# Kernel optimization log

Measured on AMD Instinct MI355X. Metric: run time of the kernel, lower is better.

The kernel has to match this reference:

```python
import jax, jax.numpy as jnp
import numpy as np

# Fixed architecture constants (from DMGHAN.__init__ / Mamba defaults)
D_MODEL = 256; D_STATE = 16; D_CONV = 4; D_INNER = 512; DT_RANK = 16
EMBED = 1024; N_CLASSES = [5, 30, 80, 200, 600, 1500]
B, L = 8, 2048


def setup_inputs() -> dict:
    key = jax.random.key(0)
    ks = jax.random.split(key, 32)
    def p(i, shape, s=0.02):
        return jax.random.normal(ks[i], shape, jnp.float32) * s
    inp = {
        "x": jax.random.normal(ks[0], (B, L, EMBED), jnp.float32),
        # input_proj
        "W_proj": p(1, (D_MODEL, EMBED)), "b_proj": p(2, (D_MODEL,)),
        # Mamba block params
        "W_in": p(3, (2 * D_INNER, D_MODEL)),
        "conv_w": p(4, (D_INNER, 1, D_CONV), 0.1), "conv_b": p(5, (D_INNER,), 0.1),
        "W_xp": p(6, (DT_RANK + 2 * D_STATE, D_INNER)),
        "W_dt": p(7, (D_INNER, DT_RANK), 0.1), "b_dt": p(8, (D_INNER,), 0.1),
        "A_log": jnp.log(jnp.broadcast_to(jnp.arange(1., D_STATE + 1., dtype=jnp.float32), (D_INNER, D_STATE))),
        "Dp": jnp.ones((D_INNER,), jnp.float32),
        "W_out": p(9, (D_MODEL, D_INNER)),
        # 6 MultiheadAttention layers (in_proj packed [q;k;v], out_proj)
        "mha_in_w": p(10, (6, 3 * D_MODEL, D_MODEL)), "mha_in_b": p(11, (6, 3 * D_MODEL)),
        "mha_out_w": p(12, (6, D_MODEL, D_MODEL)), "mha_out_b": p(13, (6, D_MODEL)),
        # 5 gates: Linear(512, 256) + sigmoid
        "gate_w": p(14, (5, D_MODEL, 2 * D_MODEL)), "gate_b": p(15, (5, D_MODEL)),
    }
    for i, nc in enumerate(N_CLASSES):
        inp[f"Wc{i}"] = p(16 + i, (nc, D_MODEL))
        inp[f"bc{i}"] = p(22 + i, (nc,))
    return inp


def mamba_block(x, W_in, conv_w, conv_b, W_xp, W_dt, b_dt, A_log, Dp, W_out):
    # x: (B, L, D_MODEL)
    u, z = jnp.split(x @ W_in.T, 2, axis=-1)          # each (B, L, D_INNER)
    # causal depthwise conv over time
    uc = jax.lax.conv_general_dilated(
        u.transpose(0, 2, 1), conv_w, window_strides=(1,),
        padding=[(D_CONV - 1, 0)], dimension_numbers=('NCH', 'OIH', 'NCH'),
        feature_group_count=D_INNER)
    u = jax.nn.silu(uc.transpose(0, 2, 1) + conv_b)    # (B, L, D_INNER)
    xdbc = u @ W_xp.T                                  # (B, L, DT_RANK + 2*N)
    dt = jax.nn.softplus(xdbc[..., :DT_RANK] @ W_dt.T + b_dt)   # (B, L, D_INNER)
    Bm = xdbc[..., DT_RANK:DT_RANK + D_STATE]          # (B, L, N)
    Cm = xdbc[..., DT_RANK + D_STATE:]                 # (B, L, N)
    A = -jnp.exp(A_log)                                # (D_INNER, N)

    def step(h, inp):
        d_t, B_t, C_t, u_t = inp                       # (B,D_INNER),(B,N),(B,N),(B,D_INNER)
        h = jnp.exp(d_t[..., None] * A) * h + (d_t * u_t)[..., None] * B_t[:, None, :]
        y = jnp.einsum('bdn,bn->bd', h, C_t)
        return h, y

    h0 = jnp.zeros((x.shape[0], D_INNER, D_STATE), x.dtype)
    xs = (dt.transpose(1, 0, 2), Bm.transpose(1, 0, 2), Cm.transpose(1, 0, 2), u.transpose(1, 0, 2))
    _, ys = jax.lax.scan(step, h0, xs)                 # ys: (L, B, D_INNER)
    y = ys.transpose(1, 0, 2) + u * Dp
    y = y * jax.nn.silu(z)
    return y @ W_out.T                                 # (B, L, D_MODEL)


def reference(x, W_proj, b_proj, W_in, conv_w, conv_b, W_xp, W_dt, b_dt, A_log, Dp, W_out,
              mha_in_w, mha_in_b, mha_out_w, mha_out_b, gate_w, gate_b,
              Wc0, bc0, Wc1, bc1, Wc2, bc2, Wc3, bc3, Wc4, bc4, Wc5, bc5):
    h = x @ W_proj.T + b_proj                          # (B, L, 256)
    seq = mamba_block(h, W_in, conv_w, conv_b, W_xp, W_dt, b_dt, A_log, Dp, W_out)
    pooled = seq.mean(axis=1)                          # (B, 256)

    feats = []
    cur = None
    for i in range(6):
        if i == 0:
            f = pooled
        else:
            g = jax.nn.sigmoid(jnp.concatenate([cur, pooled], -1) @ gate_w[i - 1].T + gate_b[i - 1])
            f = g * cur + (1. - g) * pooled
        # MHA self-attention with seq_len=1: softmax over a single key is identically 1,
        # so attn_out = out_proj(v_proj(f)) exactly (same value AND gradients).
        v = f @ mha_in_w[i][2 * D_MODEL:].T + mha_in_b[i][2 * D_MODEL:]
        cur = v @ mha_out_w[i].T + mha_out_b[i]
        feats.append(cur)

    Wcs = [Wc0, Wc1, Wc2, Wc3, Wc4, Wc5]
    bcs = [bc0, bc1, bc2, bc3, bc4, bc5]
    return tuple(f @ W.T + b for f, W, b in zip(feats, Wcs, bcs))
```

## Files before the change

kernel.cpp:

```cpp
#include <hip/hip_runtime.h>
#include <stdint.h>

typedef unsigned short u16;
typedef uint32_t u32;
typedef __attribute__((ext_vector_type(8))) short bf16x8;
typedef __attribute__((ext_vector_type(4))) float f32x4;

__device__ __forceinline__ float bf2f(u16 u){ return __uint_as_float(((u32)u) << 16); }
__device__ __forceinline__ u16 f2bf(float f){
    u32 u = __float_as_uint(f);
    u += 0x7FFFu + ((u >> 16) & 1u);
    return (u16)(u >> 16);
}

#define AS1(p) ((const __attribute__((address_space(1))) void*)(p))
#define AS3(p) ((__attribute__((address_space(3))) void*)(p))

#define HW_GATE 0
#define HW_WV   655360
#define HW_WO   1048576
#define HW_TOT  1441792

__global__ __launch_bounds__(256)
void convert_x(const float* __restrict__ xsrc, u16* __restrict__ dst)
{
    const int i = (blockIdx.x*256 + threadIdx.x)*8;
    const float4 a = *(const float4*)(xsrc + i);
    const float4 b = *(const float4*)(xsrc + i + 4);
    ushort4 o0; o0.x=f2bf(a.x); o0.y=f2bf(a.y); o0.z=f2bf(a.z); o0.w=f2bf(a.w);
    ushort4 o1; o1.x=f2bf(b.x); o1.y=f2bf(b.y); o1.z=f2bf(b.z); o1.w=f2bf(b.w);
    *(ushort4*)(dst+i) = o0; *(ushort4*)(dst+i+4) = o1;
}

__global__ __launch_bounds__(256)
void convert_w(const float* __restrict__ W_proj, const float* __restrict__ W_in,
               const float* __restrict__ W_xp,  const float* __restrict__ gate_w,
               const float* __restrict__ mha_in_w, const float* __restrict__ mha_out_w,
               u16* __restrict__ wproj, u16* __restrict__ win,
               u16* __restrict__ wxpp,  u16* __restrict__ whead)
{
    const int gid = blockIdx.x*256 + threadIdx.x;
    if(gid < 262144){
        wproj[gid] = f2bf(W_proj[gid]);
    } else if(gid < 786432){
        const int g = gid - 262144;
        win[g] = f2bf(W_in[g]);
    } else if(gid < 851968){
        const int g = gid - 786432;
        wxpp[g] = ((g >> 9) < 48) ? f2bf(W_xp[g]) : (u16)0;
    } else if(gid < 1507328){
        const int g = gid - 851968;
        whead[HW_GATE + g] = f2bf(gate_w[g]);
    } else if(gid < 1900544){
        const int g = gid - 1507328;
        const int i = g >> 16, rk = g & 65535;
        whead[HW_WV + g] = f2bf(mha_in_w[(size_t)i*196608 + 131072 + rk]);
    } else if(gid < 2293760){
        const int g = gid - 1900544;
        whead[HW_WO + g] = f2bf(mha_out_w[g]);
    }
}

template<int EPI>
__global__ __launch_bounds__(256)
void gemm_bt(const u16* __restrict__ A, const u16* __restrict__ B,
             const float* __restrict__ bias, u16* __restrict__ C,
             int K, int lda, int ldb, int ldc, int nTilesN)
{
    __shared__ __align__(16) u16 As[128*32];
    __shared__ __align__(16) u16 Bs[128*32];
    const int tid  = threadIdx.x;
    const int bm   = blockIdx.x / nTilesN, bn = blockIdx.x % nTilesN;
    const int m0   = bm*128, n0 = bn*128;
    const int lane = tid & 63, wave = tid >> 6;
    const int r1 = tid >> 2,        p1 = tid & 3;
    const int r2 = (tid+256) >> 2,  p2 = (tid+256) & 3;
    const u16* gA1 = A + (size_t)(m0 + r1)*lda + p1*8;
    const u16* gA2 = A + (size_t)(m0 + r2)*lda + p2*8;
    const u16* gB1 = B + (size_t)(n0 + r1)*ldb + p1*8;
    const u16* gB2 = B + (size_t)(n0 + r2)*ldb + p2*8;
    u16* lA1 = As + wave*512;
    u16* lA2 = As + 2048 + wave*512;
    u16* lB1 = Bs + wave*512;
    u16* lB2 = Bs + 2048 + wave*512;

    f32x4 acc[4][4];
    #pragma unroll
    for(int i=0;i<4;i++)
        #pragma unroll
        for(int j=0;j<4;j++) acc[i][j] = (f32x4){0.f,0.f,0.f,0.f};

    const int wm = (wave>>1)*64, wn = (wave&1)*64;
    const int fr = lane & 15, fq = lane >> 4;

    for(int k0 = 0; k0 < K; k0 += 32){
        __syncthreads();
        __builtin_amdgcn_global_load_lds(AS1(gA1 + k0), AS3(lA1), 16, 0, 0);
        __builtin_amdgcn_global_load_lds(AS1(gA2 + k0), AS3(lA2), 16, 0, 0);
        __builtin_amdgcn_global_load_lds(AS1(gB1 + k0), AS3(lB1), 16, 0, 0);
        __builtin_amdgcn_global_load_lds(AS1(gB2 + k0), AS3(lB2), 16, 0, 0);
        __syncthreads();
        bf16x8 af[4], bw[4];
        #pragma unroll
        for(int i=0;i<4;i++){
            af[i] = *(const bf16x8*)(As + (wm + 16*i + fr)*32 + fq*8);
            bw[i] = *(const bf16x8*)(Bs + (wn + 16*i + fr)*32 + fq*8);
        }
        #pragma unroll
        for(int i=0;i<4;i++)
            #pragma unroll
            for(int j=0;j<4;j++)
                acc[i][j] = __builtin_amdgcn_mfma_f32_16x16x32_bf16(af[i], bw[j], acc[i][j], 0,0,0);
    }

    const int mbase = m0 + wm + fq*4;
    #pragma unroll
    for(int j=0;j<4;j++){
        const int ncol = n0 + wn + 16*j + fr;
        const float bv = (EPI >= 1) ? bias[ncol] : 0.f;
        #pragma unroll
        for(int i=0;i<4;i++){
            #pragma unroll
            for(int r=0;r<4;r++){
                C[(size_t)(mbase + 16*i + r)*ldc + ncol] = f2bf(acc[i][j][r] + bv);
            }
        }
    }
}

__global__ __launch_bounds__(256)
void dt_kernel(const u16* __restrict__ xdbc, const float* __restrict__ W_dt,
               const float* __restrict__ b_dt, u16* __restrict__ dtb)
{
    const int m0 = blockIdx.x*64;
    const int d0 = threadIdx.x;
    float w0[16], w1[16];
    #pragma unroll
    for(int k=0;k<16;k++){ w0[k]=W_dt[d0*16+k]; w1[k]=W_dt[(d0+256)*16+k]; }
    const float bb0=b_dt[d0], bb1=b_dt[d0+256];
    for(int r=0;r<64;r++){
        const int m=m0+r;
        float xv[16];
        #pragma unroll
        for(int k=0;k<16;k++) xv[k]=bf2f(xdbc[(size_t)m*128+k]);
        float a0=bb0, a1=bb1;
        #pragma unroll
        for(int k=0;k<16;k++){ a0+=xv[k]*w0[k]; a1+=xv[k]*w1[k]; }
        a0 = (a0>15.f)? a0 : __logf(1.f+__expf(a0));
        a1 = (a1>15.f)? a1 : __logf(1.f+__expf(a1));
        dtb[(size_t)m*512+d0]     = f2bf(a0);
        dtb[(size_t)m*512+d0+256] = f2bf(a1);
    }
}

__global__ __launch_bounds__(256)
void conv_silu(const u16* __restrict__ xin, const float* __restrict__ conv_w,
               const float* __restrict__ conv_b, u16* __restrict__ u2)
{
    const int idx = blockIdx.x*256 + threadIdx.x;
    const int d = idx & 511;
    const int m = idx >> 9;
    const int l = m & 2047;
    const u16* base = xin + (size_t)m*1024 + d;
    float acc = conv_b[d];
    const float w0 = conv_w[d*4+0];
    const float w1 = conv_w[d*4+1];
    const float w2 = conv_w[d*4+2];
    const float w3 = conv_w[d*4+3];
    if(l >= 3) acc += bf2f(base[-3*1024])*w0;
    if(l >= 2) acc += bf2f(base[-2*1024])*w1;
    if(l >= 1) acc += bf2f(base[-1*1024])*w2;
    acc += bf2f(base[0])*w3;
    u2[idx] = f2bf(acc / (1.f + __expf(-acc)));
}

__global__ __launch_bounds__(512)
void scan_a(const u16* __restrict__ dtb, const u16* __restrict__ u2,
            const u16* __restrict__ xdbc, const float* __restrict__ A_log,
            float* __restrict__ P, float* __restrict__ S)
{
    const int b = blockIdx.x >> 5, c = blockIdx.x & 31;
    const int d = threadIdx.x;
    const int m0 = b*2048 + c*64;
    __shared__ float Bsh[64][16];
    for(int i = d; i < 1024; i += 512){
        const int tt = i >> 4, n = i & 15;
        Bsh[tt][n] = bf2f(xdbc[(size_t)(m0+tt)*128 + 16 + n]);
    }
    __syncthreads();
    float An[16];
    #pragma unroll
    for(int n=0;n<16;n++) An[n] = -__expf(A_log[d*16+n]);
    float h[16];
    #pragma unroll
    for(int n=0;n<16;n++) h[n] = 0.f;
    float dts = 0.f;
    for(int t=0;t<64;t++){
        const int m = m0 + t;
        const float dtv = bf2f(dtb[(size_t)m*512 + d]);
        const float uv  = bf2f(u2[(size_t)m*512 + d]);
        const float du  = dtv*uv;
        dts += dtv;
        #pragma unroll
        for(int n=0;n<16;n++){
            h[n] = __expf(An[n]*dtv)*h[n] + du*Bsh[t][n];
        }
    }
    const size_t o = ((size_t)(b*32 + c)*512 + d)*16;
    #pragma unroll
    for(int n=0;n<16;n++){ P[o+n] = __expf(An[n]*dts); S[o+n] = h[n]; }
}

__global__ __launch_bounds__(256)
void scan_b(const float* __restrict__ P, const float* __restrict__ S,
            float* __restrict__ Hin)
{
    const int gid = blockIdx.x*256 + threadIdx.x;
    const int b = gid >> 13;
    const int dn = gid & 8191;
    float h = 0.f;
    for(int c=0;c<32;c++){
        const size_t o = (size_t)(b*32 + c)*8192 + dn;
        const float t = P[o]*h + S[o];
        Hin[o] = h;
        h = t;
    }
}

__global__ __launch_bounds__(512)
void scan_c(const u16* __restrict__ dtb, const u16* __restrict__ u2,
            const u16* __restrict__ xdbc, const u16* __restrict__ xin,
            const float* __restrict__ A_log, const float* __restrict__ Dp,
            const float* __restrict__ Hin, float* __restrict__ ypc)
{
    const int b = blockIdx.x >> 5, c = blockIdx.x & 31;
    const int d = threadIdx.x;
    const int m0 = b*2048 + c*64;
    __shared__ float Bsh[64][16];
    __shared__ float Csh[64][16];
    for(int i = d; i < 1024; i += 512){
        const int tt = i >> 4, n = i & 15;
        const size_t row = (size_t)(m0+tt)*128;
        Bsh[tt][n] = bf2f(xdbc[row + 16 + n]);
        Csh[tt][n] = bf2f(xdbc[row + 32 + n]);
    }
    __syncthreads();
    float An[16];
    #pragma unroll
    for(int n=0;n<16;n++) An[n] = -__expf(A_log[d*16+n]);
    const float Dpd = Dp[d];
    const size_t ho = ((size_t)(b*32 + c)*512 + d)*16;
    float h[16];
    #pragma unroll
    for(int n=0;n<16;n++) h[n] = Hin[ho+n];
    float ysum = 0.f;
    for(int t=0;t<64;t++){
        const int m = m0 + t;
        const float dtv = bf2f(dtb[(size_t)m*512 + d]);
        const float uv  = bf2f(u2[(size_t)m*512 + d]);
        const float du  = dtv*uv;
        float y = 0.f;
        #pragma unroll
        for(int n=0;n<16;n++){
            h[n] = __expf(An[n]*dtv)*h[n] + du*Bsh[t][n];
            y += h[n]*Csh[t][n];
        }
        y += uv*Dpd;
        const float zv = bf2f(xin[(size_t)m*1024 + 512 + d]);
        y *= zv / (1.f + __expf(-zv));
        ysum += y;
    }
    ypc[(size_t)(b*32 + c)*512 + d] = ysum;
}

__global__ __launch_bounds__(256)
void pool_proj(const float* __restrict__ ypc, const float* __restrict__ W_out,
               float* __restrict__ pooled)
{
    __shared__ float yp[512];
    const int b = blockIdx.x, m = threadIdx.x;
    for(int d = m; d < 512; d += 256){
        float s = 0.f;
        for(int c=0;c<32;c++) s += ypc[(size_t)(b*32 + c)*512 + d];
        yp[d] = s;
    }
    __syncthreads();
    const float* w = W_out + (size_t)m*512;
    float s = 0.f;
    for(int d=0; d<512; d++) s += yp[d]*w[d];
    pooled[b*256 + m] = s*(1.f/2048.f);
}

__global__ __launch_bounds__(1024)
void head_chain(const float* __restrict__ pooled, const u16* __restrict__ whead,
                const float* __restrict__ mha_in_b, const float* __restrict__ mha_out_b,
                const float* __restrict__ gate_b, float* __restrict__ feats)
{
    constexpr int S1 = 520, S2 = 264;
    __shared__ __align__(16) u16 A1[16*S1];
    __shared__ __align__(16) u16 A2[16*S2];
    __shared__ __align__(16) u16 A3[16*S2];
    __shared__ float pl[2048], cl[2048];
    const int tid = threadIdx.x, lane = tid & 63, wave = tid >> 6;
    const int fr = lane & 15, fq = lane >> 4;
    const int wn = wave*16;
    const int nn = wn + fr;

    for(int i=tid;i<2048;i+=1024) pl[i] = pooled[i];
    for(int i=tid;i<16*S2;i+=1024){
        const int bi = i/S2, n = i - bi*S2;
        A2[i] = f2bf((bi<8 && n<256) ? pooled[bi*256+n] : 0.f);
    }
    for(int i=tid;i<16*S1;i+=1024) A1[i] = 0;
    __syncthreads();

    for(int st=0; st<6; ++st){
        if(st>0){
            for(int i=tid;i<8*S1;i+=1024){
                const int bi = i/S1, n = i - bi*S1;
                float v = 0.f;
                if(n<256)      v = cl[bi*256+n];
                else if(n<512) v = pl[bi*256+(n-256)];
                A1[i] = f2bf(v);
            }
            __syncthreads();
            const u16* gw = whead + HW_GATE + (size_t)(st-1)*131072
                          + (size_t)nn*512 + fq*8;
            bf16x8 bw[16];
            #pragma unroll
            for(int i=0;i<16;i++) bw[i] = *(const bf16x8*)(gw + i*32);
            f32x4 acc = (f32x4){0.f,0.f,0.f,0.f};
            #pragma unroll
            for(int i=0;i<16;i++){
                const bf16x8 af = *(const bf16x8*)(A1 + fr*S1 + i*32 + fq*8);
                acc = __builtin_amdgcn_mfma_f32_16x16x32_bf16(af, bw[i], acc, 0,0,0);
            }
            const float gbv = gate_b[(st-1)*256 + nn];
            #pragma unroll
            for(int r=0;r<4;r++){
                const int bi = fq*4 + r;
                if(bi<8){
                    const float g = 1.f/(1.f + __expf(-(acc[r] + gbv)));
                    A2[bi*S2 + nn] = f2bf(g*cl[bi*256+nn] + (1.f-g)*pl[bi*256+nn]);
                }
            }
            __syncthreads();
        }
        {
            const u16* wv = whead + HW_WV + (size_t)st*65536 + (size_t)nn*256 + fq*8;
            bf16x8 bw[8];
            #pragma unroll
            for(int i=0;i<8;i++) bw[i] = *(const bf16x8*)(wv + i*32);
            f32x4 acc = (f32x4){0.f,0.f,0.f,0.f};
            #pragma unroll
            for(int i=0;i<8;i++){
                const bf16x8 af = *(const bf16x8*)(A2 + fr*S2 + i*32 + fq*8);
                acc = __builtin_amdgcn_mfma_f32_16x16x32_bf16(af, bw[i], acc, 0,0,0);
            }
            const float bvv = mha_in_b[st*768 + 512 + nn];
            #pragma unroll
            for(int r=0;r<4;r++){
                const int bi = fq*4 + r;
                A3[bi*S2 + nn] = f2bf(bi<8 ? acc[r] + bvv : 0.f);
            }
            __syncthreads();
        }
        {
            const u16* wo = whead + HW_WO + (size_t)st*65536 + (size_t)nn*256 + fq*8;
            bf16x8 bw[8];
            #pragma unroll
            for(int i=0;i<8;i++) bw[i] = *(const bf16x8*)(wo + i*32);
            f32x4 acc = (f32x4){0.f,0.f,0.f,0.f};
            #pragma unroll
            for(int i=0;i<8;i++){
                const bf16x8 af = *(const bf16x8*)(A3 + fr*S2 + i*32 + fq*8);
                acc = __builtin_amdgcn_mfma_f32_16x16x32_bf16(af, bw[i], acc, 0,0,0);
            }
            const float bov = mha_out_b[st*256 + nn];
            #pragma unroll
            for(int r=0;r<4;r++){
                const int bi = fq*4 + r;
                if(bi<8){
                    const float cv = acc[r] + bov;
                    cl[bi*256 + nn] = cv;
                    feats[(size_t)st*2048 + bi*256 + nn] = cv;
                }
            }
            __syncthreads();
        }
    }
}

__global__ __launch_bounds__(256)
void classifier_k(const float* __restrict__ feats,
    const float* __restrict__ W0, const float* __restrict__ b0,
    const float* __restrict__ W1, const float* __restrict__ b1,
    const float* __restrict__ W2, const float* __restrict__ b2,
    const float* __restrict__ W3, const float* __restrict__ b3,
    const float* __restrict__ W4, const float* __restrict__ b4,
    const float* __restrict__ W5, const float* __restrict__ b5,
    float* __restrict__ out)
{
    const int tid = blockIdx.x*256 + threadIdx.x;
    if(tid >= 19320) return;
    const int b  = tid & 7;
    const int ic = tid >> 3;
    int i, c, nc, ooff;
    const float *W, *bb;
    if(ic < 5)       { i=0; c=ic;      nc=5;    ooff=0;    W=W0; bb=b0; }
    else if(ic<35)   { i=1; c=ic-5;    nc=30;   ooff=40;   W=W1; bb=b1; }
    else if(ic<115)  { i=2; c=ic-35;   nc=80;   ooff=280;  W=W2; bb=b2; }
    else if(ic<315)  { i=3; c=ic-115;  nc=200;  ooff=920;  W=W3; bb=b3; }
    else if(ic<915)  { i=4; c=ic-315;  nc=600;  ooff=2520; W=W4; bb=b4; }
    else             { i=5; c=ic-915;  nc=1500; ooff=7320; W=W5; bb=b5; }
    const float* f = feats + ((size_t)i*8 + b)*256;
    const float* w = W + (size_t)c*256;
    float acc = bb[c];
    for(int m=0;m<256;m++) acc += f[m]*w[m];
    out[ooff + b*nc + c] = acc;
}

extern "C" void kernel_launch(void* const* d_in, const int* in_sizes, int n_in,
                              void* d_out, int out_size, void* d_ws, size_t ws_size,
                              hipStream_t stream)
{
    const float* x         = (const float*)d_in[0];
    const float* W_proj    = (const float*)d_in[1];
    const float* b_proj    = (const float*)d_in[2];
    const float* W_in      = (const float*)d_in[3];
    const float* conv_w    = (const float*)d_in[4];
    const float* conv_b    = (const float*)d_in[5];
    const float* W_xp      = (const float*)d_in[6];
    const float* W_dt      = (const float*)d_in[7];
    const float* b_dt      = (const float*)d_in[8];
    const float* A_log     = (const float*)d_in[9];
    const float* Dp        = (const float*)d_in[10];
    const float* W_out     = (const float*)d_in[11];
    const float* mha_in_w  = (const float*)d_in[12];
    const float* mha_in_b  = (const float*)d_in[13];
    const float* mha_out_w = (const float*)d_in[14];
    const float* mha_out_b = (const float*)d_in[15];
    const float* gate_w    = (const float*)d_in[16];
    const float* gate_b    = (const float*)d_in[17];

    char* ws = (char*)d_ws;
    u16*   xbf    = (u16*)  (ws + 0);
    u16*   xin    = (u16*)  (ws + 0);
    u16*   h      = (u16*)  (ws + 33554432);
    float* P      = (float*)(ws + 33554432);
    u16*   u2     = (u16*)  (ws + 41943040);
    u16*   xdbc   = (u16*)  (ws + 58720256);
    u16*   dtb    = (u16*)  (ws + 62914560);
    float* S      = (float*)(ws + 79691776);
    float* Hin    = (float*)(ws + 88080384);
    float* ypc    = (float*)(ws + 96468992);
    float* pooled = (float*)(ws + 96993280);
    float* feats  = (float*)(ws + 97001472);
    u16*   wproj  = (u16*)  (ws + 97058816);
    u16*   win    = (u16*)  (ws + 97583104);
    u16*   wxpp   = (u16*)  (ws + 98631680);
    u16*   whead  = (u16*)  (ws + 98762752);

    convert_x<<<dim3(8192), 256, 0, stream>>>(x, xbf);
    convert_w<<<dim3(8960), 256, 0, stream>>>(W_proj, W_in, W_xp, gate_w,
                                              mha_in_w, mha_out_w,
                                              wproj, win, wxpp, whead);

    gemm_bt<1><<<dim3(128*2), 256, 0, stream>>>(xbf, wproj, b_proj, h,
        1024, 1024, 1024, 256, 2);
    gemm_bt<0><<<dim3(128*8), 256, 0, stream>>>(h, win, nullptr, xin,
        256, 256, 256, 1024, 8);
    conv_silu<<<dim3(32768), 256, 0, stream>>>(xin, conv_w, conv_b, u2);
    gemm_bt<0><<<dim3(128), 256, 0, stream>>>(u2, wxpp, nullptr, xdbc,
        512, 512, 512, 128, 1);
    dt_kernel<<<dim3(256), 256, 0, stream>>>(xdbc, W_dt, b_dt, dtb);

    scan_a<<<dim3(256), 512, 0, stream>>>(dtb, u2, xdbc, A_log, P, S);
    scan_b<<<dim3(256), 256, 0, stream>>>(P, S, Hin);
    scan_c<<<dim3(256), 512, 0, stream>>>(dtb, u2, xdbc, xin, A_log, Dp, Hin, ypc);

    pool_proj<<<dim3(8), 256, 0, stream>>>(ypc, W_out, pooled);

    head_chain<<<dim3(1), 1024, 0, stream>>>(pooled, whead, mha_in_b, mha_out_b,
                                             gate_b, feats);

    classifier_k<<<dim3(76), 256, 0, stream>>>(feats,
        (const float*)d_in[18], (const float*)d_in[19],
        (const float*)d_in[20], (const float*)d_in[21],
        (const float*)d_in[22], (const float*)d_in[23],
        (const float*)d_in[24], (const float*)d_in[25],
        (const float*)d_in[26], (const float*)d_in[27],
        (const float*)d_in[28], (const float*)d_in[29],
        (float*)d_out);
}
```

Baseline: 507.4 us.

## Fold V/out projections into one matrix and spread head chain across blocks

```diff
diff --git a/kernel.cpp b/kernel.cpp
--- a/kernel.cpp
+++ b/kernel.cpp
@@ -17,9 +17,12 @@
 #define AS3(p) ((__attribute__((address_space(3))) void*)(p))
 
 #define HW_GATE 0
-#define HW_WV   655360
+#define HW_WVT  655360
 #define HW_WO   1048576
-#define HW_TOT  1441792
+#define HW_WOV  1441792
+#define HW_TOT  1835008
+
+#define NBLK 16
 
 __global__ __launch_bounds__(256)
 void convert_x(const float* __restrict__ xsrc, u16* __restrict__ dst)
@@ -53,8 +56,8 @@
         whead[HW_GATE + g] = f2bf(gate_w[g]);
     } else if(gid < 1900544){
         const int g = gid - 1507328;
-        const int i = g >> 16, rk = g & 65535;
-        whead[HW_WV + g] = f2bf(mha_in_w[(size_t)i*196608 + 131072 + rk]);
+        const int i = g >> 16, k = (g >> 8) & 255, j = g & 255;
+        whead[HW_WVT + g] = f2bf(mha_in_w[(size_t)i*196608 + 131072 + (size_t)j*256 + k]);
     } else if(gid < 2293760){
         const int g = gid - 1900544;
         whead[HW_WO + g] = f2bf(mha_out_w[g]);
@@ -129,6 +132,87 @@
 }
 
 __global__ __launch_bounds__(256)
+void wov_k(u16* __restrict__ whead)
+{
+    __shared__ __align__(16) u16 As[128*32];
+    __shared__ __align__(16) u16 Bs[128*32];
+    const int tid  = threadIdx.x;
+    const int st   = blockIdx.x >> 2;
+    const int tile = blockIdx.x & 3;
+    const int m0   = (tile>>1)*128, n0 = (tile&1)*128;
+    const u16* A = whead + HW_WO  + (size_t)st*65536;
+    const u16* B = whead + HW_WVT + (size_t)st*65536;
+    u16*       C = whead + HW_WOV + (size_t)st*65536;
+    const int lane = tid & 63, wave = tid >> 6;
+    const int r1 = tid >> 2,        p1 = tid & 3;
+    const int r2 = (tid+256) >> 2,  p2 = (tid+256) & 3;
+    const u16* gA1 = A + (size_t)(m0 + r1)*256 + p1*8;
+    const u16* gA2 = A + (size_t)(m0 + r2)*256 + p2*8;
+    const u16* gB1 = B + (size_t)(n0 + r1)*256 + p1*8;
+    const u16* gB2 = B + (size_t)(n0 + r2)*256 + p2*8;
+    u16* lA1 = As + wave*512;
+    u16* lA2 = As + 2048 + wave*512;
+    u16* lB1 = Bs + wave*512;
+    u16* lB2 = Bs + 2048 + wave*512;
+
+    f32x4 acc[4][4];
+    #pragma unroll
+    for(int i=0;i<4;i++)
+        #pragma unroll
+        for(int j=0;j<4;j++) acc[i][j] = (f32x4){0.f,0.f,0.f,0.f};
+
+    const int wm = (wave>>1)*64, wn = (wave&1)*64;
+    const int fr = lane & 15, fq = lane >> 4;
+
+    for(int k0 = 0; k0 < 256; k0 += 32){
+        __syncthreads();
+        __builtin_amdgcn_global_load_lds(AS1(gA1 + k0), AS3(lA1), 16, 0, 0);
+        __builtin_amdgcn_global_load_lds(AS1(gA2 + k0), AS3(lA2), 16, 0, 0);
+        __builtin_amdgcn_global_load_lds(AS1(gB1 + k0), AS3(lB1), 16, 0, 0);
+        __builtin_amdgcn_global_load_lds(AS1(gB2 + k0), AS3(lB2), 16, 0, 0);
+        __syncthreads();
+        bf16x8 af[4], bw[4];
+        #pragma unroll
+        for(int i=0;i<4;i++){
+            af[i] = *(const bf16x8*)(As + (wm + 16*i + fr)*32 + fq*8);
+            bw[i] = *(const bf16x8*)(Bs + (wn + 16*i + fr)*32 + fq*8);
+        }
+        #pragma unroll
+        for(int i=0;i<4;i++)
+            #pragma unroll
+            for(int j=0;j<4;j++)
+                acc[i][j] = __builtin_amdgcn_mfma_f32_16x16x32_bf16(af[i], bw[j], acc[i][j], 0,0,0);
+    }
+
+    const int mbase = m0 + wm + fq*4;
+    #pragma unroll
+    for(int j=0;j<4;j++){
+        const int ncol = n0 + wn + 16*j + fr;
+        #pragma unroll
+        for(int i=0;i<4;i++){
+            #pragma unroll
+            for(int r=0;r<4;r++){
+                C[(size_t)(mbase + 16*i + r)*256 + ncol] = f2bf(acc[i][j][r]);
+            }
+        }
+    }
+}
+
+__global__ __launch_bounds__(256)
+void bcomb_k(const float* __restrict__ mha_out_w, const float* __restrict__ mha_in_b,
+             const float* __restrict__ mha_out_b, float* __restrict__ bcomb)
+{
+    const int st = blockIdx.x, n = threadIdx.x;
+    __shared__ float bv[256];
+    bv[n] = mha_in_b[st*768 + 512 + n];
+    __syncthreads();
+    const float* w = mha_out_w + (size_t)st*65536 + (size_t)n*256;
+    float s = mha_out_b[st*256 + n];
+    for(int k=0;k<256;k++) s += w[k]*bv[k];
+    bcomb[st*256 + n] = s;
+}
+
+__global__ __launch_bounds__(256)
 void dt_kernel(const u16* __restrict__ xdbc, const float* __restrict__ W_dt,
                const float* __restrict__ b_dt, u16* __restrict__ dtb)
 {
@@ -231,7 +315,7 @@
 void scan_c(const u16* __restrict__ dtb, const u16* __restrict__ u2,
             const u16* __restrict__ xdbc, const u16* __restrict__ xin,
             const float* __restrict__ A_log, const float* __restrict__ Dp,
-            const float* __restrict__ Hin, float* __restrict__ ypc)
+            const float* __restrict__ Hin, float* __restrict__ ysumG)
 {
     const int b = blockIdx.x >> 5, c = blockIdx.x & 31;
     const int d = threadIdx.x;
@@ -270,124 +354,165 @@
         y *= zv / (1.f + __expf(-zv));
         ysum += y;
     }
-    ypc[(size_t)(b*32 + c)*512 + d] = ysum;
-}
-
-__global__ __launch_bounds__(256)
-void pool_proj(const float* __restrict__ ypc, const float* __restrict__ W_out,
-               float* __restrict__ pooled)
-{
-    __shared__ float yp[512];
-    const int b = blockIdx.x, m = threadIdx.x;
-    for(int d = m; d < 512; d += 256){
-        float s = 0.f;
-        for(int c=0;c<32;c++) s += ypc[(size_t)(b*32 + c)*512 + d];
-        yp[d] = s;
-    }
+    atomicAdd(&ysumG[b*512 + d], ysum);
+}
+
+__device__ __forceinline__ void gridbar(unsigned* cnt, int ep)
+{
     __syncthreads();
-    const float* w = W_out + (size_t)m*512;
-    float s = 0.f;
-    for(int d=0; d<512; d++) s += yp[d]*w[d];
-    pooled[b*256 + m] = s*(1.f/2048.f);
-}
-
-__global__ __launch_bounds__(1024)
-void head_chain(const float* __restrict__ pooled, const u16* __restrict__ whead,
-                const float* __restrict__ mha_in_b, const float* __restrict__ mha_out_b,
-                const float* __restrict__ gate_b, float* __restrict__ feats)
-{
-    constexpr int S1 = 520, S2 = 264;
-    __shared__ __align__(16) u16 A1[16*S1];
-    __shared__ __align__(16) u16 A2[16*S2];
-    __shared__ __align__(16) u16 A3[16*S2];
-    __shared__ float pl[2048], cl[2048];
-    const int tid = threadIdx.x, lane = tid & 63, wave = tid >> 6;
+    if(threadIdx.x == 0){
+        __threadfence();
+        __hip_atomic_fetch_add(cnt, 1u, __ATOMIC_RELEASE, __HIP_MEMORY_SCOPE_AGENT);
+        const unsigned tgt = (unsigned)(NBLK*ep);
+        while(__hip_atomic_load(cnt, __ATOMIC_RELAXED, __HIP_MEMORY_SCOPE_AGENT) < tgt)
+            __builtin_amdgcn_s_sleep(2);
+        __threadfence();
+    }
+    __syncthreads();
+}
+
+__global__ __launch_bounds__(256)
+void head_coop(const float* __restrict__ ysumG, const float* __restrict__ W_out,
+               const u16* __restrict__ whead, const float* __restrict__ bcomb,
+               const float* __restrict__ gate_b,
+               u16* __restrict__ plA, u16* __restrict__ clA, u16* __restrict__ vA,
+               float* __restrict__ feats, unsigned* cnt)
+{
+    __shared__ float pscr[2048];
+    __shared__ float plL[128], clL[128];
+    __shared__ float PgL[768];
+    const int tid  = threadIdx.x;
+    const int nb0  = blockIdx.x*16;
+    const int lane = tid & 63, wave = tid >> 6;
     const int fr = lane & 15, fq = lane >> 4;
-    const int wn = wave*16;
-    const int nn = wn + fr;
-
-    for(int i=tid;i<2048;i+=1024) pl[i] = pooled[i];
-    for(int i=tid;i<16*S2;i+=1024){
-        const int bi = i/S2, n = i - bi*S2;
-        A2[i] = f2bf((bi<8 && n<256) ? pooled[bi*256+n] : 0.f);
-    }
-    for(int i=tid;i<16*S1;i+=1024) A1[i] = 0;
-    __syncthreads();
-
-    for(int st=0; st<6; ++st){
-        if(st>0){
-            for(int i=tid;i<8*S1;i+=1024){
-                const int bi = i/S1, n = i - bi*S1;
-                float v = 0.f;
-                if(n<256)      v = cl[bi*256+n];
-                else if(n<512) v = pl[bi*256+(n-256)];
-                A1[i] = f2bf(v);
-            }
-            __syncthreads();
-            const u16* gw = whead + HW_GATE + (size_t)(st-1)*131072
-                          + (size_t)nn*512 + fq*8;
-            bf16x8 bw[16];
-            #pragma unroll
-            for(int i=0;i<16;i++) bw[i] = *(const bf16x8*)(gw + i*32);
+    const int nn = nb0 + fr;
+    int ep = 0;
+
+    {
+        const int col16 = tid >> 4, seg = tid & 15;
+        float part[8];
+        #pragma unroll
+        for(int b=0;b<8;b++) part[b] = 0.f;
+        const float* wrow = W_out + (size_t)(nb0 + col16)*512 + seg*32;
+        const float* ys   = ysumG + seg*32;
+        for(int dd=0; dd<32; dd++){
+            const float w = wrow[dd];
+            #pragma unroll
+            for(int b=0;b<8;b++) part[b] += ys[b*512 + dd]*w;
+        }
+        #pragma unroll
+        for(int b=0;b<8;b++) pscr[(seg*16 + col16)*8 + b] = part[b];
+        __syncthreads();
+        if(tid < 128){
+            const int b = tid & 7, c16 = tid >> 3;
+            float s = 0.f;
+            for(int g=0; g<16; g++) s += pscr[(g*16 + c16)*8 + b];
+            s *= (1.f/2048.f);
+            plL[b*16 + c16] = s;
+            plA[b*256 + nb0 + c16] = f2bf(s);
+        } else {
+            const int idx = tid - 128, r = 8 + (idx >> 4), c = idx & 15;
+            const int off = r*256 + nb0 + c;
+            plA[off] = 0; clA[off] = 0; vA[off] = 0;
+        }
+    }
+    gridbar(cnt, ++ep);
+
+    if(wave == 0){
+        bf16x8 af[8];
+        #pragma unroll
+        for(int i=0;i<8;i++) af[i] = *(const bf16x8*)(plA + fr*256 + i*32 + fq*8);
+        {
+            const u16* wb = whead + HW_WOV + (size_t)nn*256 + fq*8;
+            bf16x8 bw[8];
+            #pragma unroll
+            for(int i=0;i<8;i++) bw[i] = *(const bf16x8*)(wb + i*32);
             f32x4 acc = (f32x4){0.f,0.f,0.f,0.f};
             #pragma unroll
-            for(int i=0;i<16;i++){
-                const bf16x8 af = *(const bf16x8*)(A1 + fr*S1 + i*32 + fq*8);
-                acc = __builtin_amdgcn_mfma_f32_16x16x32_bf16(af, bw[i], acc, 0,0,0);
-            }
-            const float gbv = gate_b[(st-1)*256 + nn];
+            for(int i=0;i<8;i++)
+                acc = __builtin_amdgcn_mfma_f32_16x16x32_bf16(af[i], bw[i], acc, 0,0,0);
+            const float bc = bcomb[nn];
             #pragma unroll
             for(int r=0;r<4;r++){
                 const int bi = fq*4 + r;
-                if(bi<8){
-                    const float g = 1.f/(1.f + __expf(-(acc[r] + gbv)));
-                    A2[bi*S2 + nn] = f2bf(g*cl[bi*256+nn] + (1.f-g)*pl[bi*256+nn]);
+                if(bi < 8){
+                    const float cv = acc[r] + bc;
+                    clL[bi*16 + fr] = cv;
+                    clA[bi*256 + nn] = f2bf(cv);
+                    feats[bi*256 + nn] = cv;
                 }
             }
-            __syncthreads();
-        }
-        {
-            const u16* wv = whead + HW_WV + (size_t)st*65536 + (size_t)nn*256 + fq*8;
+        }
+        #pragma unroll
+        for(int st=1; st<6; st++){
+            const u16* wb = whead + HW_GATE + (size_t)(st-1)*131072
+                          + (size_t)nn*512 + 256 + fq*8;
             bf16x8 bw[8];
             #pragma unroll
-            for(int i=0;i<8;i++) bw[i] = *(const bf16x8*)(wv + i*32);
+            for(int i=0;i<8;i++) bw[i] = *(const bf16x8*)(wb + i*32);
             f32x4 acc = (f32x4){0.f,0.f,0.f,0.f};
             #pragma unroll
-            for(int i=0;i<8;i++){
-                const bf16x8 af = *(const bf16x8*)(A2 + fr*S2 + i*32 + fq*8);
-                acc = __builtin_amdgcn_mfma_f32_16x16x32_bf16(af, bw[i], acc, 0,0,0);
-            }
-            const float bvv = mha_in_b[st*768 + 512 + nn];
+            for(int i=0;i<8;i++)
+                acc = __builtin_amdgcn_mfma_f32_16x16x32_bf16(af[i], bw[i], acc, 0,0,0);
+            const float gb = gate_b[(st-1)*256 + nn];
             #pragma unroll
             for(int r=0;r<4;r++){
                 const int bi = fq*4 + r;
-                A3[bi*S2 + nn] = f2bf(bi<8 ? acc[r] + bvv : 0.f);
+                if(bi < 8) PgL[st*128 + bi*16 + fr] = acc[r] + gb;
             }
-            __syncthreads();
-        }
-        {
-            const u16* wo = whead + HW_WO + (size_t)st*65536 + (size_t)nn*256 + fq*8;
-            bf16x8 bw[8];
-            #pragma unroll
-            for(int i=0;i<8;i++) bw[i] = *(const bf16x8*)(wo + i*32);
+        }
+    }
+    gridbar(cnt, ++ep);
+
+    for(int st=1; st<6; st++){
+        if(wave == 0){
+            const u16* wb = whead + HW_GATE + (size_t)(st-1)*131072
+                          + (size_t)nn*512 + fq*8;
+            bf16x8 af[8], bw[8];
+            #pragma unroll
+            for(int i=0;i<8;i++) bw[i] = *(const bf16x8*)(wb + i*32);
+            #pragma unroll
+            for(int i=0;i<8;i++) af[i] = *(const bf16x8*)(clA + fr*256 + i*32 + fq*8);
             f32x4 acc = (f32x4){0.f,0.f,0.f,0.f};
             #pragma unroll
-            for(int i=0;i<8;i++){
-                const bf16x8 af = *(const bf16x8*)(A3 + fr*S2 + i*32 + fq*8);
-                acc = __builtin_amdgcn_mfma_f32_16x16x32_bf16(af, bw[i], acc, 0,0,0);
-            }
-            const float bov = mha_out_b[st*256 + nn];
+            for(int i=0;i<8;i++)
+                acc = __builtin_amdgcn_mfma_f32_16x16x32_bf16(af[i], bw[i], acc, 0,0,0);
             #pragma unroll
             for(int r=0;r<4;r++){
                 const int bi = fq*4 + r;
-                if(bi<8){
-                    const float cv = acc[r] + bov;
-                    cl[bi*256 + nn] = cv;
+                if(bi < 8){
+                    const float t = acc[r] + PgL[st*128 + bi*16 + fr];
+                    const float g = 1.f/(1.f + __expf(-t));
+                    const float f = g*clL[bi*16 + fr] + (1.f - g)*plL[bi*16 + fr];
+                    vA[bi*256 + nn] = f2bf(f);
+                }
+            }
+        }
+        gridbar(cnt, ++ep);
+        if(wave == 0){
+            const u16* wb = whead + HW_WOV + (size_t)st*65536 + (size_t)nn*256 + fq*8;
+            bf16x8 af[8], bw[8];
+            #pragma unroll
+            for(int i=0;i<8;i++) bw[i] = *(const bf16x8*)(wb + i*32);
+            #pragma unroll
+            for(int i=0;i<8;i++) af[i] = *(const bf16x8*)(vA + fr*256 + i*32 + fq*8);
+            f32x4 acc = (f32x4){0.f,0.f,0.f,0.f};
+            #pragma unroll
+            for(int i=0;i<8;i++)
+                acc = __builtin_amdgcn_mfma_f32_16x16x32_bf16(af[i], bw[i], acc, 0,0,0);
+            const float bc = bcomb[st*256 + nn];
+            #pragma unroll
+            for(int r=0;r<4;r++){
+                const int bi = fq*4 + r;
+                if(bi < 8){
+                    const float cv = acc[r] + bc;
+                    clL[bi*16 + fr] = cv;
+                    clA[bi*256 + nn] = f2bf(cv);
                     feats[(size_t)st*2048 + bi*256 + nn] = cv;
                 }
             }
-            __syncthreads();
-        }
+        }
+        if(st < 5) gridbar(cnt, ++ep);
     }
 }
 
@@ -453,18 +578,26 @@
     u16*   dtb    = (u16*)  (ws + 62914560);
     float* S      = (float*)(ws + 79691776);
     float* Hin    = (float*)(ws + 88080384);
-    float* ypc    = (float*)(ws + 96468992);
-    float* pooled = (float*)(ws + 96993280);
+    float* ysumG  = (float*)(ws + 96468992);
+    unsigned* cnt = (unsigned*)(ws + 96468992 + 16384);
+    u16*   plA    = (u16*)  (ws + 96468992 + 16640);
+    u16*   clA    = (u16*)  (ws + 96468992 + 24832);
+    u16*   vA     = (u16*)  (ws + 96468992 + 33024);
     float* feats  = (float*)(ws + 97001472);
     u16*   wproj  = (u16*)  (ws + 97058816);
     u16*   win    = (u16*)  (ws + 97583104);
     u16*   wxpp   = (u16*)  (ws + 98631680);
     u16*   whead  = (u16*)  (ws + 98762752);
+    float* bcomb  = (float*)(ws + 102432768);
+
+    hipMemsetAsync(ws + 96468992, 0, 16448, stream);
 
     convert_x<<<dim3(8192), 256, 0, stream>>>(x, xbf);
     convert_w<<<dim3(8960), 256, 0, stream>>>(W_proj, W_in, W_xp, gate_w,
                                               mha_in_w, mha_out_w,
                                               wproj, win, wxpp, whead);
+    wov_k<<<dim3(24), 256, 0, stream>>>(whead);
+    bcomb_k<<<dim3(6), 256, 0, stream>>>(mha_out_w, mha_in_b, mha_out_b, bcomb);
 
     gemm_bt<1><<<dim3(128*2), 256, 0, stream>>>(xbf, wproj, b_proj, h,
         1024, 1024, 1024, 256, 2);
@@ -477,12 +610,10 @@
 
     scan_a<<<dim3(256), 512, 0, stream>>>(dtb, u2, xdbc, A_log, P, S);
     scan_b<<<dim3(256), 256, 0, stream>>>(P, S, Hin);
-    scan_c<<<dim3(256), 512, 0, stream>>>(dtb, u2, xdbc, xin, A_log, Dp, Hin, ypc);
-
-    pool_proj<<<dim3(8), 256, 0, stream>>>(ypc, W_out, pooled);
-
-    head_chain<<<dim3(1), 1024, 0, stream>>>(pooled, whead, mha_in_b, mha_out_b,
-                                             gate_b, feats);
+    scan_c<<<dim3(256), 512, 0, stream>>>(dtb, u2, xdbc, xin, A_log, Dp, Hin, ysumG);
+
+    head_coop<<<dim3(NBLK), 256, 0, stream>>>(ysumG, W_out, whead, bcomb,
+                                              gate_b, plA, clA, vA, feats, cnt);
 
     classifier_k<<<dim3(76), 256, 0, stream>>>(feats,
         (const float*)d_in[18], (const float*)d_in[19],
```

Result: faster. 462.2 us (-8.9%).
